# Kernel tuning notes

Measured on AMD Instinct MI355X. Metric: run time of the kernel, lower is better.

## Reference

```python
import jax, jax.numpy as jnp
import numpy as np

B, D, E, K, H = 16384, 4096, 64, 8, 128


def setup_inputs() -> dict:
    key = jax.random.key(0)
    ks = jax.random.split(key, 6)
    return {
        "r_pooled": jax.random.normal(ks[0], (B, D), jnp.float32),
        "step_frac": jnp.asarray(0.37, jnp.float32),
        "hidden_norm": jax.random.uniform(ks[1], (B,), jnp.float32),
        "confidence": jax.random.uniform(ks[2], (B,), jnp.float32),
        # params stored (in, out); equivalent math to torch Linear
        "W1": jax.random.normal(ks[3], (D + 3, H), jnp.float32) / np.sqrt(D + 3),
        "b1": jnp.zeros((H,), jnp.float32),
        "W2": jax.random.normal(ks[4], (H, E), jnp.float32) / np.sqrt(H),
        "b2": jnp.zeros((E,), jnp.float32),
    }


def reference(r_pooled, step_frac, hidden_norm, confidence, W1, b1, W2, b2):
    b = r_pooled.shape[0]
    step_col = step_frac * jnp.ones((b, 1), r_pooled.dtype)  # torch.full((B,1), step_frac)
    features = jnp.concatenate(
        [r_pooled, step_col, hidden_norm[:, None], confidence[:, None]], axis=-1
    )  # (B, D+3)
    h = jax.nn.silu(features @ W1 + b1)          # (B, 128)
    logits = h @ W2 + b2                         # (B, E)
    topk_vals, topk_idx = jax.lax.top_k(logits, K)
    topk_weights = jax.nn.softmax(topk_vals, axis=-1)
    weights = jnp.zeros_like(logits).at[jnp.arange(b)[:, None], topk_idx].set(topk_weights)
    return weights, logits
```

## Files before the change

### kernel.cpp

```cpp
#include <hip/hip_runtime.h>
#include <math.h>

#define DGL 4096
#define HGL 128
#define EGL 64
#define DELTA 5e-4f

typedef short  short8 __attribute__((ext_vector_type(8)));
typedef float  f32x4  __attribute__((ext_vector_type(4)));

__device__ inline unsigned short bf16_rne(float x) {
    unsigned u = __float_as_uint(x);
    u += 0x7FFFu + ((u >> 16) & 1u);
    return (unsigned short)(u >> 16);
}
__device__ inline void split2(float x, short& hi, short& lo) {
    unsigned u = __float_as_uint(x);
    hi = (short)(u >> 16);
    float hif = __uint_as_float(u & 0xFFFF0000u);
    lo = (short)bf16_rne(x - hif);
}
__device__ inline void split8(const float* f, short8& hi, short8& lo) {
#pragma unroll
    for (int j = 0; j < 8; ++j) { short h, l2; split2(f[j], h, l2); hi[j] = h; lo[j] = l2; }
}

__global__ void pack_w1(const float* __restrict__ W1, unsigned short* __restrict__ wsB1) {
    const int b = blockIdx.x;
    const int kci = b >> 3, nt = b & 7;
    const int l = threadIdx.x, quad = l >> 4, l15 = l & 15;
    short8 vh, vl;
#pragma unroll
    for (int j = 0; j < 8; ++j) {
        const int k = kci * 32 + quad * 8 + j;
        short h, lo; split2(W1[(size_t)k * HGL + nt * 16 + l15], h, lo);
        vh[j] = h; vl[j] = lo;
    }
    *(short8*)(wsB1 + (size_t)kci * 8192 + ((nt * 2 + 0) * 64 + l) * 8) = vh;
    *(short8*)(wsB1 + (size_t)kci * 8192 + ((nt * 2 + 1) * 64 + l) * 8) = vl;
}

__global__ void pack_w2(const float* __restrict__ W2, unsigned short* __restrict__ wsB2,
                        int* __restrict__ gcount) {
    if (blockIdx.x == 0 && threadIdx.x == 0) *gcount = 0;
    const int b = blockIdx.x;
    const int kc2 = b >> 2, nt = b & 3;
    const int l = threadIdx.x, quad = l >> 4, l15 = l & 15;
    short8 vh, vl;
#pragma unroll
    for (int j = 0; j < 8; ++j) {
        const int k = kc2 * 32 + quad * 8 + j;
        short h, lo; split2(W2[k * EGL + nt * 16 + l15], h, lo);
        vh[j] = h; vl[j] = lo;
    }
    *(short8*)(wsB2 + ((kc2 * 4 + nt) * 2 + 0) * 512 + l * 8) = vh;
    *(short8*)(wsB2 + ((kc2 * 4 + nt) * 2 + 1) * 512 + l * 8) = vl;
}

__global__ __launch_bounds__(64, 1) void router_main(
    const float* __restrict__ r_pooled, const float* __restrict__ step_frac,
    const float* __restrict__ hn, const float* __restrict__ cf,
    const float* __restrict__ W1, const float* __restrict__ b1,
    const float* __restrict__ b2v,
    const unsigned short* __restrict__ wsB1, const unsigned short* __restrict__ wsB2,
    int* __restrict__ gcount, int* __restrict__ glist,
    float* __restrict__ out_w, float* __restrict__ out_l)
{
    __shared__ float hs[32 * 132];
    __shared__ float ls[32 * 65];
    __shared__ float wt[32 * 65];

    const int l = threadIdx.x;
    const int quad = l >> 4, l15 = l & 15;
    const int row0 = blockIdx.x * 32;

    const float* aB0 = r_pooled + (size_t)(row0 + l15) * DGL + quad * 8;
    const float* aB1 = aB0 + (size_t)16 * DGL;

    f32x4 acc[2][8];
#pragma unroll
    for (int m = 0; m < 2; ++m)
#pragma unroll
        for (int nt = 0; nt < 8; ++nt) acc[m][nt] = (f32x4){0.f, 0.f, 0.f, 0.f};

    float4 a0[4];
    a0[0] = *(const float4*)(aB0);
    a0[1] = *(const float4*)(aB0 + 4);
    a0[2] = *(const float4*)(aB1);
    a0[3] = *(const float4*)(aB1 + 4);

    for (int kci = 0; kci < 128; ++kci) {
        const int kn = (kci + 1 < 128) ? (kci + 1) : 127;
        float4 a1[4];
        a1[0] = *(const float4*)(aB0 + kn * 32);
        a1[1] = *(const float4*)(aB0 + kn * 32 + 4);
        a1[2] = *(const float4*)(aB1 + kn * 32);
        a1[3] = *(const float4*)(aB1 + kn * 32 + 4);

        const unsigned short* bp = wsB1 + (size_t)kci * 8192 + l * 8;
        short8 b[16];
#pragma unroll
        for (int nt = 0; nt < 8; ++nt) {
            b[2 * nt]     = *(const short8*)(bp + (2 * nt) * 512);
            b[2 * nt + 1] = *(const short8*)(bp + (2 * nt + 1) * 512);
        }

        short8 ahi[2], alo[2];
#pragma unroll
        for (int m = 0; m < 2; ++m) {
            float fa[8];
#pragma unroll
            for (int j = 0; j < 4; ++j) { fa[j] = a0[2 * m][j]; fa[j + 4] = a0[2 * m + 1][j]; }
            split8(fa, ahi[m], alo[m]);
        }
#pragma unroll
        for (int m = 0; m < 2; ++m)
#pragma unroll
            for (int nt = 0; nt < 8; ++nt) {
                acc[m][nt] = __builtin_amdgcn_mfma_f32_16x16x32_bf16(ahi[m], b[2 * nt],     acc[m][nt], 0, 0, 0);
                acc[m][nt] = __builtin_amdgcn_mfma_f32_16x16x32_bf16(ahi[m], b[2 * nt + 1], acc[m][nt], 0, 0, 0);
                acc[m][nt] = __builtin_amdgcn_mfma_f32_16x16x32_bf16(alo[m], b[2 * nt],     acc[m][nt], 0, 0, 0);
            }
#pragma unroll
        for (int i = 0; i < 4; ++i) a0[i] = a1[i];
    }

    {
        const float sf = step_frac[0];
        float hnv[8], cfv[8];
#pragma unroll
        for (int m = 0; m < 2; ++m)
#pragma unroll
            for (int r = 0; r < 4; ++r) {
                const int row = row0 + m * 16 + quad * 4 + r;
                hnv[m * 4 + r] = hn[row];
                cfv[m * 4 + r] = cf[row];
            }
#pragma unroll
        for (int nt = 0; nt < 8; ++nt) {
            const int c = nt * 16 + l15;
            const float w96 = W1[(size_t)4096 * HGL + c];
            const float w97 = W1[(size_t)4097 * HGL + c];
            const float w98 = W1[(size_t)4098 * HGL + c];
            const float bb  = b1[c];
#pragma unroll
            for (int m = 0; m < 2; ++m)
#pragma unroll
                for (int r = 0; r < 4; ++r) {
                    const float x = acc[m][nt][r] + sf * w96 + hnv[m * 4 + r] * w97
                                  + cfv[m * 4 + r] * w98 + bb;
                    hs[(m * 16 + quad * 4 + r) * 132 + c] = x / (1.0f + expf(-x));
                }
        }
    }
    __syncthreads();

    f32x4 acc2[2][4];
#pragma unroll
    for (int m = 0; m < 2; ++m)
#pragma unroll
        for (int nt = 0; nt < 4; ++nt) acc2[m][nt] = (f32x4){0.f, 0.f, 0.f, 0.f};

#pragma unroll
    for (int kc2 = 0; kc2 < 4; ++kc2) {
        const unsigned short* bp2 = wsB2 + kc2 * 4096 + l * 8;
        short8 c2[8];
#pragma unroll
        for (int nt = 0; nt < 4; ++nt) {
            c2[2 * nt]     = *(const short8*)(bp2 + (2 * nt) * 512);
            c2[2 * nt + 1] = *(const short8*)(bp2 + (2 * nt + 1) * 512);
        }
#pragma unroll
        for (int m = 0; m < 2; ++m) {
            const float4 va = *(const float4*)&hs[(m * 16 + l15) * 132 + kc2 * 32 + quad * 8];
            const float4 vb = *(const float4*)&hs[(m * 16 + l15) * 132 + kc2 * 32 + quad * 8 + 4];
            float fa[8];
#pragma unroll
            for (int j = 0; j < 4; ++j) { fa[j] = ((const float*)&va)[j]; fa[j + 4] = ((const float*)&vb)[j]; }
            short8 h2, lo2v;
            split8(fa, h2, lo2v);
#pragma unroll
            for (int nt = 0; nt < 4; ++nt) {
                acc2[m][nt] = __builtin_amdgcn_mfma_f32_16x16x32_bf16(h2,   c2[2 * nt],     acc2[m][nt], 0, 0, 0);
                acc2[m][nt] = __builtin_amdgcn_mfma_f32_16x16x32_bf16(h2,   c2[2 * nt + 1], acc2[m][nt], 0, 0, 0);
                acc2[m][nt] = __builtin_amdgcn_mfma_f32_16x16x32_bf16(lo2v, c2[2 * nt],     acc2[m][nt], 0, 0, 0);
            }
        }
    }

#pragma unroll
    for (int m = 0; m < 2; ++m)
#pragma unroll
        for (int nt = 0; nt < 4; ++nt) {
            const int c = nt * 16 + l15;
            const float bv = b2v[c];
#pragma unroll
            for (int r = 0; r < 4; ++r) {
                const int lr = m * 16 + quad * 4 + r;
                const float v = acc2[m][nt][r] + bv;
                out_l[(size_t)(row0 + lr) * EGL + c] = v;
                ls[lr * 65 + c] = v;
            }
        }
    for (int i = l; i < 32 * 65; i += 64) wt[i] = 0.0f;
    __syncthreads();

    if (l < 32) {
        float vals[9]; int idxs[9];
#pragma unroll
        for (int i = 0; i < 9; ++i) { vals[i] = -INFINITY; idxs[i] = 0; }
        for (int e = 0; e < EGL; ++e) {
            const float v = ls[l * 65 + e];
            if (v > vals[8]) {
                int p = 8;
                while (p > 0 && v > vals[p - 1]) { vals[p] = vals[p - 1]; idxs[p] = idxs[p - 1]; --p; }
                vals[p] = v; idxs[p] = e;
            }
        }
        const float mx = vals[0];
        float wgt[8], ssum = 0.0f;
#pragma unroll
        for (int i = 0; i < 8; ++i) { wgt[i] = expf(vals[i] - mx); ssum += wgt[i]; }
        const float inv = 1.0f / ssum;
#pragma unroll
        for (int i = 0; i < 8; ++i) wt[l * 65 + idxs[i]] = wgt[i] * inv;
        if (vals[7] - vals[8] < DELTA) {
            int p = atomicAdd(gcount, 1);
            if (p < 16384) glist[p] = row0 + l;
        }
    }
    __syncthreads();

    for (int i = l; i < 32 * EGL; i += 64) {
        const int m = i >> 6, c = i & 63;
        out_w[(size_t)(row0 + m) * EGL + c] = wt[m * 65 + c];
    }
}

__global__ __launch_bounds__(512, 1) void refine_rows(
    const float* __restrict__ r_pooled, const float* __restrict__ step_frac,
    const float* __restrict__ hn, const float* __restrict__ cf,
    const float* __restrict__ W1, const float* __restrict__ b1,
    const float* __restrict__ W2, const float* __restrict__ b2,
    const int* __restrict__ gcount, const int* __restrict__ glist,
    float* __restrict__ out_w)
{
    __shared__ __align__(16) float als[DGL];
    __shared__ float part[4][128];
    __shared__ float hred[128];
    __shared__ float lb[64];
    __shared__ float wb[64];

    const int t = threadIdx.x;
    const int cnt = *gcount;
    const int c = t & 127, sl = t >> 7;

    for (int i = blockIdx.x; i < cnt; i += gridDim.x) {
        const int row = glist[i];
        __syncthreads();
        for (int j = t; j < DGL / 4; j += 512)
            *(float4*)&als[j * 4] = *(const float4*)&r_pooled[(size_t)row * DGL + j * 4];
        __syncthreads();

        float pr = 0.0f;
        const float* ap = als + sl * 1024;
        const float* wp = W1 + (size_t)(sl * 1024) * HGL + c;
#pragma unroll 8
        for (int k = 0; k < 1024; ++k) pr = fmaf(ap[k], wp[(size_t)k * HGL], pr);
        part[sl][c] = pr;
        __syncthreads();

        if (t < 128) {
            const float sf = step_frac[0];
            float x = part[0][t] + part[1][t] + part[2][t] + part[3][t];
            x += sf * W1[(size_t)4096 * HGL + t] + hn[row] * W1[(size_t)4097 * HGL + t]
               + cf[row] * W1[(size_t)4098 * HGL + t] + b1[t];
            hred[t] = x / (1.0f + expf(-x));
        }
        __syncthreads();
        if (t < 64) {
            float a = b2[t];
            for (int k = 0; k < HGL; ++k) a = fmaf(hred[k], W2[k * EGL + t], a);
            lb[t] = a; wb[t] = 0.0f;
        }
        __syncthreads();
        if (t == 0) {
            float vals[8]; int idxs[8];
#pragma unroll
            for (int q = 0; q < 8; ++q) { vals[q] = -INFINITY; idxs[q] = 0; }
            for (int e = 0; e < EGL; ++e) {
                const float v = lb[e];
                if (v > vals[7]) {
                    int p = 7;
                    while (p > 0 && v > vals[p - 1]) { vals[p] = vals[p - 1]; idxs[p] = idxs[p - 1]; --p; }
                    vals[p] = v; idxs[p] = e;
                }
            }
            const float mx = vals[0];
            float wgt[8], ssum = 0.0f;
#pragma unroll
            for (int q = 0; q < 8; ++q) { wgt[q] = expf(vals[q] - mx); ssum += wgt[q]; }
            const float inv = 1.0f / ssum;
#pragma unroll
            for (int q = 0; q < 8; ++q) wb[idxs[q]] = wgt[q] * inv;
        }
        __syncthreads();
        if (t < 64) out_w[(size_t)row * EGL + t] = wb[t];
    }
}

extern "C" void kernel_launch(void* const* d_in, const int* in_sizes, int n_in,
                              void* d_out, int out_size, void* d_ws, size_t ws_size,
                              hipStream_t stream) {
    const float* r_pooled    = (const float*)d_in[0];
    const float* step_frac   = (const float*)d_in[1];
    const float* hidden_norm = (const float*)d_in[2];
    const float* confidence  = (const float*)d_in[3];
    const float* W1          = (const float*)d_in[4];
    const float* b1          = (const float*)d_in[5];
    const float* W2          = (const float*)d_in[6];
    const float* b2          = (const float*)d_in[7];

    const int B = in_sizes[2];
    float* out_w = (float*)d_out;
    float* out_l = out_w + (size_t)B * EGL;

    unsigned short* wsB1 = (unsigned short*)d_ws;
    unsigned short* wsB2 = (unsigned short*)((char*)d_ws + 2097152);
    int* gcount = (int*)((char*)d_ws + 2129920);
    int* glist  = (int*)((char*)d_ws + 2129984);

    hipLaunchKernelGGL(pack_w1, dim3(1024), dim3(64), 0, stream, W1, wsB1);
    hipLaunchKernelGGL(pack_w2, dim3(16), dim3(64), 0, stream, W2, wsB2, gcount);
    hipLaunchKernelGGL(router_main, dim3(B / 32), dim3(64), 0, stream,
                       r_pooled, step_frac, hidden_norm, confidence,
                       W1, b1, b2, wsB1, wsB2, gcount, glist, out_w, out_l);
    hipLaunchKernelGGL(refine_rows, dim3(256), dim3(512), 0, stream,
                       r_pooled, step_frac, hidden_norm, confidence,
                       W1, b1, W2, b2, gcount, glist, out_w);
}
```

Baseline: 619.8 us.

## Split router K-loop across four waves with shared-memory reduction

Each block of the main router kernel now runs four wavefronts instead of one. Each wave handles a quarter of the 4096-long reduction dimension, and the partial accumulators are summed serially through shared memory. The SiLU epilogue and the second small GEMM are then spread across all 256 threads. This shortens the per-block serial K loop and raises latency hiding per CU, at the cost of extra barriers and a serialized shared-memory reduction.

```diff
diff --git a/kernel.cpp b/kernel.cpp
--- a/kernel.cpp
+++ b/kernel.cpp
@@ -57,7 +57,7 @@
     *(short8*)(wsB2 + ((kc2 * 4 + nt) * 2 + 1) * 512 + l * 8) = vl;
 }
 
-__global__ __launch_bounds__(64, 1) void router_main(
+__global__ __launch_bounds__(256, 2) void router_main(
     const float* __restrict__ r_pooled, const float* __restrict__ step_frac,
     const float* __restrict__ hn, const float* __restrict__ cf,
     const float* __restrict__ W1, const float* __restrict__ b1,
@@ -66,15 +66,16 @@
     int* __restrict__ gcount, int* __restrict__ glist,
     float* __restrict__ out_w, float* __restrict__ out_l)
 {
-    __shared__ float hs[32 * 132];
+    __shared__ float hsum[32 * 132];
     __shared__ float ls[32 * 65];
     __shared__ float wt[32 * 65];
 
-    const int l = threadIdx.x;
+    const int t = threadIdx.x;
+    const int w = t >> 6, l = t & 63;
     const int quad = l >> 4, l15 = l & 15;
     const int row0 = blockIdx.x * 32;
 
-    const float* aB0 = r_pooled + (size_t)(row0 + l15) * DGL + quad * 8;
+    const float* aB0 = r_pooled + (size_t)(row0 + l15) * DGL + w * 1024 + quad * 8;
     const float* aB1 = aB0 + (size_t)16 * DGL;
 
     f32x4 acc[2][8];
@@ -89,15 +90,15 @@
     a0[2] = *(const float4*)(aB1);
     a0[3] = *(const float4*)(aB1 + 4);
 
-    for (int kci = 0; kci < 128; ++kci) {
-        const int kn = (kci + 1 < 128) ? (kci + 1) : 127;
+    for (int kci = 0; kci < 32; ++kci) {
+        const int kn = (kci + 1 < 32) ? (kci + 1) : 31;
         float4 a1[4];
         a1[0] = *(const float4*)(aB0 + kn * 32);
         a1[1] = *(const float4*)(aB0 + kn * 32 + 4);
         a1[2] = *(const float4*)(aB1 + kn * 32);
         a1[3] = *(const float4*)(aB1 + kn * 32 + 4);
 
-        const unsigned short* bp = wsB1 + (size_t)kci * 8192 + l * 8;
+        const unsigned short* bp = wsB1 + (size_t)(w * 32 + kci) * 8192 + l * 8;
         short8 b[16];
 #pragma unroll
         for (int nt = 0; nt < 8; ++nt) {
@@ -125,92 +126,90 @@
         for (int i = 0; i < 4; ++i) a0[i] = a1[i];
     }
 
+    if (w == 0) {
+#pragma unroll
+        for (int m = 0; m < 2; ++m)
+#pragma unroll
+            for (int nt = 0; nt < 8; ++nt)
+#pragma unroll
+                for (int r = 0; r < 4; ++r)
+                    hsum[(m * 16 + quad * 4 + r) * 132 + nt * 16 + l15] = acc[m][nt][r];
+    }
+    __syncthreads();
+#pragma unroll
+    for (int wv = 1; wv < 4; ++wv) {
+        if (w == wv) {
+#pragma unroll
+            for (int m = 0; m < 2; ++m)
+#pragma unroll
+                for (int nt = 0; nt < 8; ++nt)
+#pragma unroll
+                    for (int r = 0; r < 4; ++r)
+                        hsum[(m * 16 + quad * 4 + r) * 132 + nt * 16 + l15] += acc[m][nt][r];
+        }
+        __syncthreads();
+    }
+
     {
         const float sf = step_frac[0];
-        float hnv[8], cfv[8];
-#pragma unroll
-        for (int m = 0; m < 2; ++m)
-#pragma unroll
-            for (int r = 0; r < 4; ++r) {
-                const int row = row0 + m * 16 + quad * 4 + r;
-                hnv[m * 4 + r] = hn[row];
-                cfv[m * 4 + r] = cf[row];
-            }
-#pragma unroll
-        for (int nt = 0; nt < 8; ++nt) {
-            const int c = nt * 16 + l15;
-            const float w96 = W1[(size_t)4096 * HGL + c];
-            const float w97 = W1[(size_t)4097 * HGL + c];
-            const float w98 = W1[(size_t)4098 * HGL + c];
-            const float bb  = b1[c];
-#pragma unroll
-            for (int m = 0; m < 2; ++m)
-#pragma unroll
-                for (int r = 0; r < 4; ++r) {
-                    const float x = acc[m][nt][r] + sf * w96 + hnv[m * 4 + r] * w97
-                                  + cfv[m * 4 + r] * w98 + bb;
-                    hs[(m * 16 + quad * 4 + r) * 132 + c] = x / (1.0f + expf(-x));
-                }
+#pragma unroll
+        for (int j = 0; j < 16; ++j) {
+            const int idx = j * 256 + t;
+            const int r = idx >> 7, c = idx & 127;
+            float x = hsum[r * 132 + c];
+            x += sf * W1[(size_t)4096 * HGL + c]
+               + hn[row0 + r] * W1[(size_t)4097 * HGL + c]
+               + cf[row0 + r] * W1[(size_t)4098 * HGL + c] + b1[c];
+            hsum[r * 132 + c] = x / (1.0f + expf(-x));
         }
     }
     __syncthreads();
 
-    f32x4 acc2[2][4];
-#pragma unroll
-    for (int m = 0; m < 2; ++m)
-#pragma unroll
-        for (int nt = 0; nt < 4; ++nt) acc2[m][nt] = (f32x4){0.f, 0.f, 0.f, 0.f};
-
+    const int mt2 = w >> 1, nh2 = w & 1;
+    f32x4 acc2[2];
+    acc2[0] = (f32x4){0.f, 0.f, 0.f, 0.f};
+    acc2[1] = (f32x4){0.f, 0.f, 0.f, 0.f};
 #pragma unroll
     for (int kc2 = 0; kc2 < 4; ++kc2) {
-        const unsigned short* bp2 = wsB2 + kc2 * 4096 + l * 8;
-        short8 c2[8];
-#pragma unroll
-        for (int nt = 0; nt < 4; ++nt) {
-            c2[2 * nt]     = *(const short8*)(bp2 + (2 * nt) * 512);
-            c2[2 * nt + 1] = *(const short8*)(bp2 + (2 * nt + 1) * 512);
-        }
-#pragma unroll
-        for (int m = 0; m < 2; ++m) {
-            const float4 va = *(const float4*)&hs[(m * 16 + l15) * 132 + kc2 * 32 + quad * 8];
-            const float4 vb = *(const float4*)&hs[(m * 16 + l15) * 132 + kc2 * 32 + quad * 8 + 4];
-            float fa[8];
-#pragma unroll
-            for (int j = 0; j < 4; ++j) { fa[j] = ((const float*)&va)[j]; fa[j + 4] = ((const float*)&vb)[j]; }
-            short8 h2, lo2v;
-            split8(fa, h2, lo2v);
-#pragma unroll
-            for (int nt = 0; nt < 4; ++nt) {
-                acc2[m][nt] = __builtin_amdgcn_mfma_f32_16x16x32_bf16(h2,   c2[2 * nt],     acc2[m][nt], 0, 0, 0);
-                acc2[m][nt] = __builtin_amdgcn_mfma_f32_16x16x32_bf16(h2,   c2[2 * nt + 1], acc2[m][nt], 0, 0, 0);
-                acc2[m][nt] = __builtin_amdgcn_mfma_f32_16x16x32_bf16(lo2v, c2[2 * nt],     acc2[m][nt], 0, 0, 0);
-            }
-        }
-    }
-
-#pragma unroll
-    for (int m = 0; m < 2; ++m)
-#pragma unroll
-        for (int nt = 0; nt < 4; ++nt) {
-            const int c = nt * 16 + l15;
-            const float bv = b2v[c];
-#pragma unroll
-            for (int r = 0; r < 4; ++r) {
-                const int lr = m * 16 + quad * 4 + r;
-                const float v = acc2[m][nt][r] + bv;
-                out_l[(size_t)(row0 + lr) * EGL + c] = v;
-                ls[lr * 65 + c] = v;
-            }
-        }
-    for (int i = l; i < 32 * 65; i += 64) wt[i] = 0.0f;
+        const float4 va = *(const float4*)&hsum[(mt2 * 16 + l15) * 132 + kc2 * 32 + quad * 8];
+        const float4 vb = *(const float4*)&hsum[(mt2 * 16 + l15) * 132 + kc2 * 32 + quad * 8 + 4];
+        float fa[8];
+#pragma unroll
+        for (int j = 0; j < 4; ++j) { fa[j] = ((const float*)&va)[j]; fa[j + 4] = ((const float*)&vb)[j]; }
+        short8 h2, lo2;
+        split8(fa, h2, lo2);
+#pragma unroll
+        for (int ntp = 0; ntp < 2; ++ntp) {
+            const int nt = nh2 * 2 + ntp;
+            const short8 bh = *(const short8*)(wsB2 + ((kc2 * 4 + nt) * 2 + 0) * 512 + l * 8);
+            const short8 bl = *(const short8*)(wsB2 + ((kc2 * 4 + nt) * 2 + 1) * 512 + l * 8);
+            acc2[ntp] = __builtin_amdgcn_mfma_f32_16x16x32_bf16(h2,  bh, acc2[ntp], 0, 0, 0);
+            acc2[ntp] = __builtin_amdgcn_mfma_f32_16x16x32_bf16(h2,  bl, acc2[ntp], 0, 0, 0);
+            acc2[ntp] = __builtin_amdgcn_mfma_f32_16x16x32_bf16(lo2, bh, acc2[ntp], 0, 0, 0);
+        }
+    }
+
+#pragma unroll
+    for (int ntp = 0; ntp < 2; ++ntp) {
+        const int c = (nh2 * 2 + ntp) * 16 + l15;
+        const float bv = b2v[c];
+#pragma unroll
+        for (int r = 0; r < 4; ++r) {
+            const int lr = mt2 * 16 + quad * 4 + r;
+            const float v = acc2[ntp][r] + bv;
+            out_l[(size_t)(row0 + lr) * EGL + c] = v;
+            ls[lr * 65 + c] = v;
+        }
+    }
+    for (int i = t; i < 32 * 65; i += 256) wt[i] = 0.0f;
     __syncthreads();
 
-    if (l < 32) {
+    if (t < 32) {
         float vals[9]; int idxs[9];
 #pragma unroll
         for (int i = 0; i < 9; ++i) { vals[i] = -INFINITY; idxs[i] = 0; }
         for (int e = 0; e < EGL; ++e) {
-            const float v = ls[l * 65 + e];
+            const float v = ls[t * 65 + e];
             if (v > vals[8]) {
                 int p = 8;
                 while (p > 0 && v > vals[p - 1]) { vals[p] = vals[p - 1]; idxs[p] = idxs[p - 1]; --p; }
@@ -223,15 +222,15 @@
         for (int i = 0; i < 8; ++i) { wgt[i] = expf(vals[i] - mx); ssum += wgt[i]; }
         const float inv = 1.0f / ssum;
 #pragma unroll
-        for (int i = 0; i < 8; ++i) wt[l * 65 + idxs[i]] = wgt[i] * inv;
+        for (int i = 0; i < 8; ++i) wt[t * 65 + idxs[i]] = wgt[i] * inv;
         if (vals[7] - vals[8] < DELTA) {
             int p = atomicAdd(gcount, 1);
-            if (p < 16384) glist[p] = row0 + l;
+            if (p < 16384) glist[p] = row0 + t;
         }
     }
     __syncthreads();
 
-    for (int i = l; i < 32 * EGL; i += 64) {
+    for (int i = t; i < 32 * EGL; i += 256) {
         const int m = i >> 6, c = i & 63;
         out_w[(size_t)(row0 + m) * EGL + c] = wt[m * 65 + c];
     }
@@ -332,7 +331,7 @@
 
     hipLaunchKernelGGL(pack_w1, dim3(1024), dim3(64), 0, stream, W1, wsB1);
     hipLaunchKernelGGL(pack_w2, dim3(16), dim3(64), 0, stream, W2, wsB2, gcount);
-    hipLaunchKernelGGL(router_main, dim3(B / 32), dim3(64), 0, stream,
+    hipLaunchKernelGGL(router_main, dim3(B / 32), dim3(256), 0, stream,
                        r_pooled, step_frac, hidden_norm, confidence,
                        W1, b1, b2, wsB1, wsB2, gcount, glist, out_w, out_l);
     hipLaunchKernelGGL(refine_rows, dim3(256), dim3(512), 0, stream,
```

Measured after the change: 562.1 us. 9.3% less time.
